# Kernel optimization log

Measured on AMD Instinct MI355X. Metric: run time of the kernel, lower is better.

The kernel has to match this reference:

```python
import jax, jax.numpy as jnp
import numpy as np

B, L, D, H = 2, 2048, 512, 8
HD = D // H
DIL, WIN, CAUSAL = 2, 256, True
HIDDEN = 4 * D
EPS = 1e-5


def _layer_norm(x, w, b):
    m = jnp.mean(x, axis=-1, keepdims=True)
    v = jnp.mean(jnp.square(x - m), axis=-1, keepdims=True)
    return (x - m) * jax.lax.rsqrt(v + EPS) * w + b


def setup_inputs() -> dict:
    key = jax.random.key(0)
    ks = jax.random.split(key, 6)
    sc = 0.02
    return {
        "x": jax.random.normal(ks[0], (B, L, D), jnp.float32),
        "norm1_w": jnp.ones((D,), jnp.float32),
        "norm1_b": jnp.zeros((D,), jnp.float32),
        "qkv_w": jax.random.normal(ks[1], (3 * D, D), jnp.float32) * sc,
        "qkv_b": jnp.zeros((3 * D,), jnp.float32),
        "out_w": jax.random.normal(ks[2], (D, D), jnp.float32) * sc,
        "out_b": jnp.zeros((D,), jnp.float32),
        "norm2_w": jnp.ones((D,), jnp.float32),
        "norm2_b": jnp.zeros((D,), jnp.float32),
        "ffn_w1": jax.random.normal(ks[3], (HIDDEN, D), jnp.float32) * sc,
        "ffn_b1": jnp.zeros((HIDDEN,), jnp.float32),
        "ffn_w2": jax.random.normal(ks[4], (D, HIDDEN), jnp.float32) * sc,
        "ffn_b2": jnp.zeros((D,), jnp.float32),
    }


def reference(x, norm1_w, norm1_b, qkv_w, qkv_b, out_w, out_b,
              norm2_w, norm2_b, ffn_w1, ffn_b1, ffn_w2, ffn_b2):
    # pre-norm attention block
    h = _layer_norm(x, norm1_w, norm1_b)                       # [B,L,D]
    qkv = h @ qkv_w.T + qkv_b                                  # [B,L,3D]
    q, k, v = jnp.split(qkv, 3, axis=-1)

    def heads(t):  # [B,L,D] -> [B,H,L,HD]
        return t.reshape(B, L, H, HD).transpose(0, 2, 1, 3)

    q, k, v = heads(q), heads(k), heads(v)

    # dilated / windowed / causal keep mask (True = attend)
    idx = jnp.arange(L)
    delta = idx[:, None] - idx[None, :]                        # [L,L]
    keep = (delta % DIL) == 0
    keep &= jnp.abs(delta) <= WIN
    if CAUSAL:
        keep &= delta >= 0

    scale = 1.0 / np.sqrt(HD)
    scores = jnp.einsum('bhqd,bhkd->bhqk', q, k) * scale       # [B,H,L,L]
    scores = jnp.where(keep, scores, jnp.finfo(scores.dtype).min)
    attn = jax.nn.softmax(scores, axis=-1)
    o = jnp.einsum('bhqk,bhkd->bhqd', attn, v)                 # [B,H,L,HD]
    o = o.transpose(0, 2, 1, 3).reshape(B, L, D)
    o = o @ out_w.T + out_b

    x = x + o                                                  # residual (dropout p=0)

    # pre-norm FFN block
    h2 = _layer_norm(x, norm2_w, norm2_b)
    f = jax.nn.gelu(h2 @ ffn_w1.T + ffn_b1, approximate=False)
    f = f @ ffn_w2.T + ffn_b2
    return x + f
```

## Files before the change

### kernel.cpp

```cpp
#include <hip/hip_runtime.h>
#include <stdint.h>

typedef float f32x4 __attribute__((ext_vector_type(4)));
typedef unsigned short u16x4 __attribute__((ext_vector_type(4)));
typedef unsigned short u16x8 __attribute__((ext_vector_type(8)));
typedef __bf16 bf16x8 __attribute__((ext_vector_type(8)));

__device__ __forceinline__ unsigned short f2bf(float f) {
  unsigned u = __float_as_uint(f);
  u += 0x7fffu + ((u >> 16) & 1u);
  return (unsigned short)(u >> 16);
}
__device__ __forceinline__ float bf2f(unsigned short h) {
  return __uint_as_float(((unsigned)h) << 16);
}
__device__ __forceinline__ f32x4 mfma16x16x32(u16x8 a, u16x8 b, f32x4 c) {
  return __builtin_amdgcn_mfma_f32_16x16x32_bf16(
      __builtin_bit_cast(bf16x8, a), __builtin_bit_cast(bf16x8, b), c, 0, 0, 0);
}
__device__ __forceinline__ void gload_lds16(const unsigned short* g, unsigned short* l) {
  __builtin_amdgcn_global_load_lds((__attribute__((address_space(1))) void*)(g),
                                   (__attribute__((address_space(3))) void*)(l), 16, 0, 0);
}

__global__ __launch_bounds__(256)
void cvt_weights(const float* __restrict__ wq, const float* __restrict__ wo,
                 const float* __restrict__ w1, const float* __restrict__ w2,
                 unsigned short* __restrict__ dst) {
  int i4 = blockIdx.x * 256 + threadIdx.x;
  int e = i4 << 2;
  const float* src; int off;
  if (e < 786432)       { src = wq; off = 0; }
  else if (e < 1048576) { src = wo; off = 786432; }
  else if (e < 2097152) { src = w1; off = 1048576; }
  else                  { src = w2; off = 2097152; }
  int le = e - off;
  f32x4 v = *(const f32x4*)(src + le);
  u16x4 o;
  #pragma unroll
  for (int i = 0; i < 4; ++i) o[i] = f2bf(v[i]);
  *(u16x4*)(dst + e) = o;
}

__global__ __launch_bounds__(256)
void ln_bf16(const float* __restrict__ x, const float* __restrict__ w,
             const float* __restrict__ b, unsigned short* __restrict__ out) {
  const int row = (blockIdx.x << 2) + (threadIdx.x >> 6);
  const int lane = threadIdx.x & 63;
  const float* xr = x + (size_t)row * 512 + (lane << 3);
  f32x4 v0 = *(const f32x4*)xr;
  f32x4 v1 = *(const f32x4*)(xr + 4);
  float s = 0.f, s2 = 0.f;
  #pragma unroll
  for (int i = 0; i < 4; ++i) { s += v0[i] + v1[i]; s2 += v0[i]*v0[i] + v1[i]*v1[i]; }
  #pragma unroll
  for (int m = 1; m < 64; m <<= 1) { s += __shfl_xor(s, m); s2 += __shfl_xor(s2, m); }
  float mean = s * (1.0f / 512.0f);
  float var  = s2 * (1.0f / 512.0f) - mean * mean;
  float rs = rsqrtf(var + 1e-5f);
  const int d = lane << 3;
  u16x8 o;
  #pragma unroll
  for (int i = 0; i < 8; ++i) {
    float xv = (i < 4) ? v0[i] : v1[i - 4];
    o[i] = f2bf((xv - mean) * rs * w[d + i] + b[d + i]);
  }
  *(u16x8*)(out + (size_t)row * 512 + d) = o;
}

template<int BM, int BN, int EPI>
__global__ __launch_bounds__(256)
void gemm_bt(const unsigned short* __restrict__ A, const unsigned short* __restrict__ B,
             const float* __restrict__ bias, const float* __restrict__ resid,
             float* __restrict__ Cf, unsigned short* __restrict__ Cb,
             int M, int N, int K) {
  constexpr int AM = BM / 32, AN = BN / 32;
  __shared__ __align__(16) unsigned short lA[BM * 64];
  __shared__ __align__(16) unsigned short lB[BN * 64];
  const int tid = threadIdx.x;
  const int wave = tid >> 6, lane = tid & 63;
  const int gn = N / BN;
  const int tm = blockIdx.x / gn, tn = blockIdx.x - tm * gn;
  const int m0 = tm * BM, n0 = tn * BN;
  const int wr = wave >> 1, wc = wave & 1;
  const int lr = lane & 15;
  const int lk = (lane >> 4) << 3;
  const int srow = tid >> 3;
  const int scol = (tid & 7) << 3;
  f32x4 acc[AM][AN] = {};
  for (int k0 = 0; k0 < K; k0 += 64) {
    #pragma unroll
    for (int it = 0; it < BM / 32; ++it)
      gload_lds16(A + (size_t)(m0 + (it << 5) + srow) * K + k0 + scol,
                  &lA[((it << 8) + (wave << 6)) << 3]);
    #pragma unroll
    for (int it = 0; it < BN / 32; ++it)
      gload_lds16(B + (size_t)(n0 + (it << 5) + srow) * K + k0 + scol,
                  &lB[((it << 8) + (wave << 6)) << 3]);
    __syncthreads();
    #pragma unroll
    for (int kk = 0; kk < 64; kk += 32) {
      u16x8 af[AM], bfv[AN];
      #pragma unroll
      for (int m = 0; m < AM; ++m)
        af[m] = *(const u16x8*)&lA[(wr * (BM / 2) + (m << 4) + lr) * 64 + kk + lk];
      #pragma unroll
      for (int n = 0; n < AN; ++n)
        bfv[n] = *(const u16x8*)&lB[(wc * (BN / 2) + (n << 4) + lr) * 64 + kk + lk];
      #pragma unroll
      for (int m = 0; m < AM; ++m)
        #pragma unroll
        for (int n = 0; n < AN; ++n)
          acc[m][n] = mfma16x16x32(af[m], bfv[n], acc[m][n]);
    }
    __syncthreads();
  }
  const int rbase = m0 + wr * (BM / 2) + ((lane >> 4) << 2);
  const int cbase = n0 + wc * (BN / 2) + lr;
  #pragma unroll
  for (int m = 0; m < AM; ++m) {
    #pragma unroll
    for (int n = 0; n < AN; ++n) {
      int col = cbase + (n << 4);
      float bcol = bias[col];
      #pragma unroll
      for (int i = 0; i < 4; ++i) {
        int row = rbase + (m << 4) + i;
        float v = acc[m][n][i] + bcol;
        size_t off = (size_t)row * N + col;
        if (EPI == 0) {
          Cb[off] = f2bf(v);
        } else if (EPI == 1) {
          Cf[off] = v + resid[off];
        } else {
          float g = 0.5f * v * (1.0f + erff(v * 0.70710678f));
          Cb[off] = f2bf(g);
        }
      }
    }
  }
}

__global__ __launch_bounds__(256)
void attn_mfma(const unsigned short* __restrict__ qkv, unsigned short* __restrict__ out) {
  __shared__ __align__(16) unsigned short Vt[64 * 216];
  __shared__ __align__(16) unsigned short Pl[4][16 * 168];
  const int bid = blockIdx.x;
  const int qt  = bid & 15;
  const int par = (bid >> 4) & 1;
  const int h   = (bid >> 5) & 7;
  const int b   = bid >> 8;
  const int q0  = qt << 6;
  const int tid = threadIdx.x, wave = tid >> 6, lane = tid & 63;

  for (int c = tid; c < 208 * 16; c += 256) {
    int r = c >> 4, dc = (c & 15) << 2;
    int kp = q0 - 128 + r;
    u16x4 vb = {0, 0, 0, 0};
    if (r < 192 && kp >= 0) {
      size_t base = ((size_t)((b << 11) + (kp << 1) + par)) * 1536 + 1024 + (h << 6) + dc;
      vb = *(const u16x4*)(qkv + base);
    }
    #pragma unroll
    for (int e = 0; e < 4; ++e) Vt[(dc + e) * 216 + r] = vb[e];
  }
  __syncthreads();

  const int col = lane & 15;
  const int rg  = lane >> 4;
  const int qt0 = q0 + (wave << 4);
  unsigned short* Pw = Pl[wave];

  const long long qrow = (long long)((b << 11) + ((qt0 + col) << 1) + par);
  const unsigned short* qp = qkv + qrow * 1536 + (h << 6) + (rg << 3);
  u16x8 qa0 = *(const u16x8*)(qp);
  u16x8 qa1 = *(const u16x8*)(qp + 32);

  f32x4 sc[9];
  #pragma unroll
  for (int j = 0; j < 9; ++j) sc[j] = (f32x4){0.f, 0.f, 0.f, 0.f};
  #pragma unroll
  for (int j = 0; j < 9; ++j) {
    int kpj = qt0 - 128 + (j << 4) + col;
    long long krow = (long long)((b << 11) + (kpj << 1) + par);
    const unsigned short* kp = qkv + krow * 1536 + 512 + (h << 6) + (rg << 3);
    u16x8 k0 = *(const u16x8*)(kp);
    u16x8 k1 = *(const u16x8*)(kp + 32);
    sc[j] = mfma16x16x32(qa0, k0, sc[j]);
    sc[j] = mfma16x16x32(qa1, k1, sc[j]);
  }

  float mrow[4] = {-3e38f, -3e38f, -3e38f, -3e38f};
  #pragma unroll
  for (int j = 0; j < 9; ++j) {
    #pragma unroll
    for (int i = 0; i < 4; ++i) {
      int qr = (rg << 2) + i;
      int jk = (j << 4) + col;
      bool ok = (jk >= qr) && (jk <= qr + 128) && (qt0 + jk >= 128);
      float s = ok ? sc[j][i] * 0.125f : -1e30f;
      sc[j][i] = s;
      mrow[i] = fmaxf(mrow[i], s);
    }
  }
  #pragma unroll
  for (int i = 0; i < 4; ++i)
    #pragma unroll
    for (int m = 1; m < 16; m <<= 1) mrow[i] = fmaxf(mrow[i], __shfl_xor(mrow[i], m));

  float lrow[4] = {0.f, 0.f, 0.f, 0.f};
  #pragma unroll
  for (int j = 0; j < 9; ++j) {
    #pragma unroll
    for (int i = 0; i < 4; ++i) {
      float p = __expf(sc[j][i] - mrow[i]);
      lrow[i] += p;
      Pw[((rg << 2) + i) * 168 + (j << 4) + col] = f2bf(p);
    }
  }
  #pragma unroll
  for (int i = 0; i < 4; ++i)
    Pw[((rg << 2) + i) * 168 + 144 + col] = 0;
  #pragma unroll
  for (int i = 0; i < 4; ++i)
    #pragma unroll
    for (int m = 1; m < 16; m <<= 1) lrow[i] += __shfl_xor(lrow[i], m);
  float inv[4];
  #pragma unroll
  for (int i = 0; i < 4; ++i) inv[i] = 1.0f / lrow[i];

  f32x4 oacc[4] = {};
  #pragma unroll
  for (int ks = 0; ks < 5; ++ks) {
    int kk = ks << 5;
    u16x8 pa = *(const u16x8*)&Pw[col * 168 + kk + (rg << 3)];
    #pragma unroll
    for (int n = 0; n < 4; ++n) {
      u16x8 vb = *(const u16x8*)&Vt[((n << 4) + col) * 216 + (wave << 4) + kk + (rg << 3)];
      oacc[n] = mfma16x16x32(pa, vb, oacc[n]);
    }
  }

  #pragma unroll
  for (int n = 0; n < 4; ++n) {
    #pragma unroll
    for (int i = 0; i < 4; ++i) {
      int q = qt0 + (rg << 2) + i;
      size_t off = ((size_t)((b << 11) + (q << 1) + par)) * 512 + (h << 6) + (n << 4) + col;
      out[off] = f2bf(oacc[n][i] * inv[i]);
    }
  }
}

extern "C" void kernel_launch(void* const* d_in, const int* in_sizes, int n_in,
                              void* d_out, int out_size, void* d_ws, size_t ws_size,
                              hipStream_t stream) {
  const float* x     = (const float*)d_in[0];
  const float* n1w   = (const float*)d_in[1];
  const float* n1b   = (const float*)d_in[2];
  const float* qkv_w = (const float*)d_in[3];
  const float* qkv_b = (const float*)d_in[4];
  const float* out_w = (const float*)d_in[5];
  const float* out_b = (const float*)d_in[6];
  const float* n2w   = (const float*)d_in[7];
  const float* n2b   = (const float*)d_in[8];
  const float* w1    = (const float*)d_in[9];
  const float* b1    = (const float*)d_in[10];
  const float* w2    = (const float*)d_in[11];
  const float* b2    = (const float*)d_in[12];

  char* ws = (char*)d_ws;
  unsigned short* wbf   = (unsigned short*)(ws);
  unsigned short* wq_bf = wbf;
  unsigned short* wo_bf = (unsigned short*)(ws + 1572864);
  unsigned short* w1_bf = (unsigned short*)(ws + 2097152);
  unsigned short* w2_bf = (unsigned short*)(ws + 4194304);
  unsigned short* h_bf  = (unsigned short*)(ws + 6291456);
  unsigned short* qkvb  = (unsigned short*)(ws + 10485760);
  unsigned short* ao_bf = (unsigned short*)(ws + 23068672);
  float*          x1    = (float*)(ws + 27262976);
  unsigned short* f1_bf = (unsigned short*)(ws + 10485760);
  float* outp = (float*)d_out;

  cvt_weights<<<3072, 256, 0, stream>>>(qkv_w, out_w, w1, w2, wbf);
  ln_bf16<<<1024, 256, 0, stream>>>(x, n1w, n1b, h_bf);
  gemm_bt<128, 64, 0><<<32 * 24, 256, 0, stream>>>(h_bf, wq_bf, qkv_b, nullptr,
                                                   nullptr, qkvb, 4096, 1536, 512);
  attn_mfma<<<512, 256, 0, stream>>>(qkvb, ao_bf);
  gemm_bt<64, 64, 1><<<64 * 8, 256, 0, stream>>>(ao_bf, wo_bf, out_b, x, x1,
                                                 nullptr, 4096, 512, 512);
  ln_bf16<<<1024, 256, 0, stream>>>(x1, n2w, n2b, h_bf);
  gemm_bt<128, 64, 2><<<32 * 32, 256, 0, stream>>>(h_bf, w1_bf, b1, nullptr,
                                                   nullptr, f1_bf, 4096, 2048, 512);
  gemm_bt<64, 64, 1><<<64 * 8, 256, 0, stream>>>(f1_bf, w2_bf, b2, x1, outp,
                                                 nullptr, 4096, 512, 2048);
}
```

Before: 104.7 us.

## Write transposed V from QKV GEMM and fuse weight conversion with first layernorm

The QKV GEMM epilogue now also writes V in a per-(batch, parity, head) transposed layout to global memory. Attention can then read its V operands straight from global instead of staging and transposing a V tile in LDS behind a block barrier. Separately, the weight bf16 conversion and the first layernorm are merged into one launch to save a kernel dispatch. The cost is that the extra transposed V stores are scattered 2-byte writes. Attention also now reads V slightly outside the valid key range at the edges and relies on zero probabilities there, where it used to zero-fill.

```diff
diff --git a/kernel.cpp b/kernel.cpp
--- a/kernel.cpp
+++ b/kernel.cpp
@@ -24,22 +24,48 @@
 }
 
 __global__ __launch_bounds__(256)
-void cvt_weights(const float* __restrict__ wq, const float* __restrict__ wo,
-                 const float* __restrict__ w1, const float* __restrict__ w2,
-                 unsigned short* __restrict__ dst) {
-  int i4 = blockIdx.x * 256 + threadIdx.x;
-  int e = i4 << 2;
-  const float* src; int off;
-  if (e < 786432)       { src = wq; off = 0; }
-  else if (e < 1048576) { src = wo; off = 786432; }
-  else if (e < 2097152) { src = w1; off = 1048576; }
-  else                  { src = w2; off = 2097152; }
-  int le = e - off;
-  f32x4 v = *(const f32x4*)(src + le);
-  u16x4 o;
-  #pragma unroll
-  for (int i = 0; i < 4; ++i) o[i] = f2bf(v[i]);
-  *(u16x4*)(dst + e) = o;
+void prep(const float* __restrict__ wq, const float* __restrict__ wo,
+          const float* __restrict__ w1, const float* __restrict__ w2,
+          unsigned short* __restrict__ dst,
+          const float* __restrict__ x, const float* __restrict__ nw,
+          const float* __restrict__ nb, unsigned short* __restrict__ hout) {
+  if (blockIdx.x < 3072) {
+    int i4 = blockIdx.x * 256 + threadIdx.x;
+    int e = i4 << 2;
+    const float* src; int off;
+    if (e < 786432)       { src = wq; off = 0; }
+    else if (e < 1048576) { src = wo; off = 786432; }
+    else if (e < 2097152) { src = w1; off = 1048576; }
+    else                  { src = w2; off = 2097152; }
+    int le = e - off;
+    f32x4 v = *(const f32x4*)(src + le);
+    u16x4 o;
+    #pragma unroll
+    for (int i = 0; i < 4; ++i) o[i] = f2bf(v[i]);
+    *(u16x4*)(dst + e) = o;
+  } else {
+    const int row = ((blockIdx.x - 3072) << 2) + (threadIdx.x >> 6);
+    const int lane = threadIdx.x & 63;
+    const float* xr = x + (size_t)row * 512 + (lane << 3);
+    f32x4 v0 = *(const f32x4*)xr;
+    f32x4 v1 = *(const f32x4*)(xr + 4);
+    float s = 0.f, s2 = 0.f;
+    #pragma unroll
+    for (int i = 0; i < 4; ++i) { s += v0[i] + v1[i]; s2 += v0[i]*v0[i] + v1[i]*v1[i]; }
+    #pragma unroll
+    for (int m = 1; m < 64; m <<= 1) { s += __shfl_xor(s, m); s2 += __shfl_xor(s2, m); }
+    float mean = s * (1.0f / 512.0f);
+    float var  = s2 * (1.0f / 512.0f) - mean * mean;
+    float rs = rsqrtf(var + 1e-5f);
+    const int d = lane << 3;
+    u16x8 o;
+    #pragma unroll
+    for (int i = 0; i < 8; ++i) {
+      float xv = (i < 4) ? v0[i] : v1[i - 4];
+      o[i] = f2bf((xv - mean) * rs * nw[d + i] + nb[d + i]);
+    }
+    *(u16x8*)(hout + (size_t)row * 512 + d) = o;
+  }
 }
 
 __global__ __launch_bounds__(256)
@@ -68,11 +94,12 @@
   *(u16x8*)(out + (size_t)row * 512 + d) = o;
 }
 
-template<int BM, int BN, int EPI>
+template<int BM, int BN, int EPI, int WRV>
 __global__ __launch_bounds__(256)
 void gemm_bt(const unsigned short* __restrict__ A, const unsigned short* __restrict__ B,
              const float* __restrict__ bias, const float* __restrict__ resid,
              float* __restrict__ Cf, unsigned short* __restrict__ Cb,
+             unsigned short* __restrict__ vt,
              int M, int N, int K) {
   constexpr int AM = BM / 32, AN = BN / 32;
   __shared__ __align__(16) unsigned short lA[BM * 64];
@@ -136,14 +163,21 @@
           float g = 0.5f * v * (1.0f + erff(v * 0.70710678f));
           Cb[off] = f2bf(g);
         }
+        if (WRV && col >= 1024) {
+          int hh = (col - 1024) >> 6, dd = (col - 1024) & 63;
+          int bb = row >> 11, tok = row & 2047;
+          long long vrow = ((((((long long)bb << 1) + (tok & 1)) << 3) + hh) << 6) + dd;
+          vt[(vrow << 10) + (tok >> 1)] = f2bf(v);
+        }
       }
     }
   }
 }
 
 __global__ __launch_bounds__(256)
-void attn_mfma(const unsigned short* __restrict__ qkv, unsigned short* __restrict__ out) {
-  __shared__ __align__(16) unsigned short Vt[64 * 216];
+void attn_mfma(const unsigned short* __restrict__ qkv,
+               const unsigned short* __restrict__ vt,
+               unsigned short* __restrict__ out) {
   __shared__ __align__(16) unsigned short Pl[4][16 * 168];
   const int bid = blockIdx.x;
   const int qt  = bid & 15;
@@ -153,19 +187,6 @@
   const int q0  = qt << 6;
   const int tid = threadIdx.x, wave = tid >> 6, lane = tid & 63;
 
-  for (int c = tid; c < 208 * 16; c += 256) {
-    int r = c >> 4, dc = (c & 15) << 2;
-    int kp = q0 - 128 + r;
-    u16x4 vb = {0, 0, 0, 0};
-    if (r < 192 && kp >= 0) {
-      size_t base = ((size_t)((b << 11) + (kp << 1) + par)) * 1536 + 1024 + (h << 6) + dc;
-      vb = *(const u16x4*)(qkv + base);
-    }
-    #pragma unroll
-    for (int e = 0; e < 4; ++e) Vt[(dc + e) * 216 + r] = vb[e];
-  }
-  __syncthreads();
-
   const int col = lane & 15;
   const int rg  = lane >> 4;
   const int qt0 = q0 + (wave << 4);
@@ -229,14 +250,17 @@
   #pragma unroll
   for (int i = 0; i < 4; ++i) inv[i] = 1.0f / lrow[i];
 
+  const long long vbase = ((long long)((((b << 1) + par) << 3) + h)) << 16;
   f32x4 oacc[4] = {};
   #pragma unroll
   for (int ks = 0; ks < 5; ++ks) {
     int kk = ks << 5;
     u16x8 pa = *(const u16x8*)&Pw[col * 168 + kk + (rg << 3)];
+    long long kp0 = (long long)qt0 - 128 + kk + (rg << 3);
     #pragma unroll
     for (int n = 0; n < 4; ++n) {
-      u16x8 vb = *(const u16x8*)&Vt[((n << 4) + col) * 216 + (wave << 4) + kk + (rg << 3)];
+      const unsigned short* vp = vt + vbase + (((long long)((n << 4) + col)) << 10) + kp0;
+      u16x8 vb = *(const u16x8*)(vp);
       oacc[n] = mfma16x16x32(pa, vb, oacc[n]);
     }
   }
@@ -280,18 +304,18 @@
   unsigned short* ao_bf = (unsigned short*)(ws + 23068672);
   float*          x1    = (float*)(ws + 27262976);
   unsigned short* f1_bf = (unsigned short*)(ws + 10485760);
+  unsigned short* vt    = (unsigned short*)(ws + 35651584);
   float* outp = (float*)d_out;
 
-  cvt_weights<<<3072, 256, 0, stream>>>(qkv_w, out_w, w1, w2, wbf);
-  ln_bf16<<<1024, 256, 0, stream>>>(x, n1w, n1b, h_bf);
-  gemm_bt<128, 64, 0><<<32 * 24, 256, 0, stream>>>(h_bf, wq_bf, qkv_b, nullptr,
-                                                   nullptr, qkvb, 4096, 1536, 512);
-  attn_mfma<<<512, 256, 0, stream>>>(qkvb, ao_bf);
-  gemm_bt<64, 64, 1><<<64 * 8, 256, 0, stream>>>(ao_bf, wo_bf, out_b, x, x1,
-                                                 nullptr, 4096, 512, 512);
+  prep<<<4096, 256, 0, stream>>>(qkv_w, out_w, w1, w2, wbf, x, n1w, n1b, h_bf);
+  gemm_bt<128, 64, 0, 1><<<32 * 24, 256, 0, stream>>>(h_bf, wq_bf, qkv_b, nullptr,
+                                                      nullptr, qkvb, vt, 4096, 1536, 512);
+  attn_mfma<<<512, 256, 0, stream>>>(qkvb, vt, ao_bf);
+  gemm_bt<64, 64, 1, 0><<<64 * 8, 256, 0, stream>>>(ao_bf, wo_bf, out_b, x, x1,
+                                                    nullptr, nullptr, 4096, 512, 512);
   ln_bf16<<<1024, 256, 0, stream>>>(x1, n2w, n2b, h_bf);
-  gemm_bt<128, 64, 2><<<32 * 32, 256, 0, stream>>>(h_bf, w1_bf, b1, nullptr,
-                                                   nullptr, f1_bf, 4096, 2048, 512);
-  gemm_bt<64, 64, 1><<<64 * 8, 256, 0, stream>>>(f1_bf, w2_bf, b2, x1, outp,
-                                                 nullptr, 4096, 512, 2048);
-}
+  gemm_bt<128, 64, 2, 0><<<32 * 32, 256, 0, stream>>>(h_bf, w1_bf, b1, nullptr,
+                                                      nullptr, f1_bf, nullptr, 4096, 2048, 512);
+  gemm_bt<64, 64, 1, 0><<<64 * 8, 256, 0, stream>>>(f1_bf, w2_bf, b2, x1, outp,
+                                                    nullptr, nullptr, 4096, 512, 2048);
+}
```

Measured after the change: 103.9 us. No clear change (-0.8%).
